# Optimization experiments

Hardware: AMD Instinct MI355X
Metric: run time of the kernel (lower is better)

The kernel has to match this reference:

```python
import jax, jax.numpy as jnp
import numpy as np

D = 512       # input_dim
K = 8         # output_size (number of bilinear slices)
L = 64        # hash_length
Q = 4096      # number of query vectors
C = 4096      # number of class vectors


def setup_inputs() -> dict:
    key = jax.random.key(0)
    ks = jax.random.split(key, 8)
    class_vector = jax.random.normal(ks[0], (C, D), dtype=jnp.float32)
    query_vector = jax.random.normal(ks[1], (Q, D), dtype=jnp.float32)
    # xavier_normal over (D, D, K): std = sqrt(2 / (fan_in + fan_out))
    xav = float(np.sqrt(2.0 / (D + D)))
    M = jax.random.normal(ks[2], (D, D, K), dtype=jnp.float32) * xav
    # score_layer: Linear(K, 1)
    lim_s = 1.0 / np.sqrt(K)
    score_w = jax.random.uniform(ks[3], (K,), jnp.float32, -lim_s, lim_s)
    score_b = jax.random.uniform(ks[4], (1,), jnp.float32, -lim_s, lim_s)
    # hash_layer: Linear(D, L) + Tanh
    lim_h = 1.0 / np.sqrt(D)
    hash_w = jax.random.uniform(ks[5], (L, D), jnp.float32, -lim_h, lim_h)
    hash_b = jax.random.uniform(ks[6], (L,), jnp.float32, -lim_h, lim_h)
    return {
        "class_vector": class_vector,
        "query_vector": query_vector,
        "M": M,
        "score_w": score_w,
        "score_b": score_b,
        "hash_w": hash_w,
        "hash_b": hash_b,
    }


def reference(class_vector, query_vector, M, score_w, score_b, hash_w, hash_b):
    # Looped bilinear product fused into one einsum:
    # inter_k = Q @ (C @ M[:,:,k]).T  ->  [Q, C, K]
    bi = jnp.einsum('ci,ijk,qj->qck', class_vector, M, query_vector)
    act = jax.nn.relu(bi)
    # score_layer: Linear(K, 1) then squeeze -> [Q, C]
    other = jnp.einsum('qck,k->qc', act, score_w) + score_b[0]
    relation_scores = jax.nn.softmax(other, axis=1)       # softmax over class dim
    query_features = relation_scores @ class_vector + query_vector  # [Q, D]
    hash_codes = jnp.tanh(query_features @ hash_w.T + hash_b)       # [Q, L]
    return hash_codes
```

## Files before the change

### kernel.cpp

```cpp
#include <hip/hip_runtime.h>
#include <hip/hip_bf16.h>
#include <math.h>

#define D_ 512
#define K_ 8
#define L_ 64
#define Q_ 4096
#define C_ 4096
#define N_ (C_ * K_)

typedef short short8 __attribute__((ext_vector_type(8)));
typedef float f32x4 __attribute__((ext_vector_type(4)));

static __device__ __forceinline__ void split2(float v, unsigned short& h, unsigned short& l) {
    __hip_bfloat16 hh = __float2bfloat16(v);
    float r = v - __bfloat162float(hh);
    __hip_bfloat16 ll = __float2bfloat16(r);
    h = *reinterpret_cast<unsigned short*>(&hh);
    l = *reinterpret_cast<unsigned short*>(&ll);
}

#define ASYNC_COPY16(gp, lp)                                                        \
    __builtin_amdgcn_global_load_lds((const __attribute__((address_space(1))) void*)(gp), \
                                     (__attribute__((address_space(3))) void*)(lp), \
                                     16, 0, 0)

__global__ void transpose_M_split(const float* __restrict__ M,
                                  unsigned short* __restrict__ Mh,
                                  unsigned short* __restrict__ Ml) {
    int idx = blockIdx.x * blockDim.x + threadIdx.x;
    int i = idx & (D_ - 1);
    int n2 = idx >> 9;
    int j = n2 & (D_ - 1);
    int k = n2 >> 9;
    float v = M[((size_t)i * D_ + j) * K_ + k];
    split2(v, Mh[idx], Ml[idx]);
}

__global__ void split_f32(const float* __restrict__ x,
                          unsigned short* __restrict__ hi,
                          unsigned short* __restrict__ lo) {
    int i = blockIdx.x * blockDim.x + threadIdx.x;
    split2(x[i], hi[i], lo[i]);
}

__global__ void transpose_split_classT(const float* __restrict__ x,
                                       unsigned short* __restrict__ Th,
                                       unsigned short* __restrict__ Tl) {
    int idx = blockIdx.x * blockDim.x + threadIdx.x;
    int c = idx & (C_ - 1);
    int d = idx >> 12;
    float v = x[(size_t)c * D_ + d];
    split2(v, Th[idx], Tl[idx]);
}

#define BM 128
#define BN 128
#define BNW 32
#define BKK 32

__device__ __forceinline__ void mfma_core(
    const unsigned short* __restrict__ Agh, const unsigned short* __restrict__ Agl,
    const unsigned short* __restrict__ Bgh, const unsigned short* __restrict__ Bgl,
    int lda, int ldb, int kd, int m0, int n0,
    unsigned short (*Ahb)[BM * BKK], unsigned short (*Alb)[BM * BKK],
    f32x4 acc[8][2]) {
    const int tid = threadIdx.x;
    const int lane = tid & 63;
    const int wid = tid >> 6;
    const int fr = lane & 15;
    const int fq = lane >> 4;
    const int co = (fq ^ ((fr >> 1) & 3)) * 8;

    const unsigned short* bh0 = Bgh + (size_t)(n0 + wid * BNW + fr) * ldb + fq * 8;
    const unsigned short* bl0 = Bgl + (size_t)(n0 + wid * BNW + fr) * ldb + fq * 8;

    short8 bh[2][2], bl[2][2];

#pragma unroll
    for (int h = 0; h < 2; ++h) {
        const int i2 = h * 256 + tid;
        const int r = i2 >> 2;
        const int cg = (i2 & 3) ^ ((r >> 1) & 3);
        const int ldsoff = (h * 256 + (tid & ~63)) * 8;
        const size_t go = (size_t)(m0 + r) * lda + cg * 8;
        ASYNC_COPY16(Agh + go, &Ahb[0][ldsoff]);
        ASYNC_COPY16(Agl + go, &Alb[0][ldsoff]);
    }
    bh[0][0] = *(const short8*)(bh0);
    bh[0][1] = *(const short8*)(bh0 + 16 * (size_t)ldb);
    bl[0][0] = *(const short8*)(bl0);
    bl[0][1] = *(const short8*)(bl0 + 16 * (size_t)ldb);
    __syncthreads();

    const int niter = kd / BKK;
#pragma unroll 2
    for (int it = 0; it < niter; ++it) {
        const int cur = it & 1, nxt = cur ^ 1;
        if (it + 1 < niter) {
            const int j0 = (it + 1) * BKK;
#pragma unroll
            for (int h = 0; h < 2; ++h) {
                const int i2 = h * 256 + tid;
                const int r = i2 >> 2;
                const int cg = (i2 & 3) ^ ((r >> 1) & 3);
                const int ldsoff = (h * 256 + (tid & ~63)) * 8;
                const size_t go = (size_t)(m0 + r) * lda + j0 + cg * 8;
                ASYNC_COPY16(Agh + go, &Ahb[nxt][ldsoff]);
                ASYNC_COPY16(Agl + go, &Alb[nxt][ldsoff]);
            }
            bh[nxt][0] = *(const short8*)(bh0 + j0);
            bh[nxt][1] = *(const short8*)(bh0 + 16 * (size_t)ldb + j0);
            bl[nxt][0] = *(const short8*)(bl0 + j0);
            bl[nxt][1] = *(const short8*)(bl0 + 16 * (size_t)ldb + j0);
        }
#pragma unroll
        for (int mi = 0; mi < 8; ++mi) {
            const short8 ah = *(const short8*)&Ahb[cur][(mi * 16 + fr) * BKK + co];
            const short8 al = *(const short8*)&Alb[cur][(mi * 16 + fr) * BKK + co];
#pragma unroll
            for (int ni = 0; ni < 2; ++ni) {
                acc[mi][ni] = __builtin_amdgcn_mfma_f32_16x16x32_bf16(ah, bh[cur][ni], acc[mi][ni], 0, 0, 0);
                acc[mi][ni] = __builtin_amdgcn_mfma_f32_16x16x32_bf16(ah, bl[cur][ni], acc[mi][ni], 0, 0, 0);
                acc[mi][ni] = __builtin_amdgcn_mfma_f32_16x16x32_bf16(al, bh[cur][ni], acc[mi][ni], 0, 0, 0);
            }
        }
        __syncthreads();
    }
}

#define CORE_PROLOGUE                                                            \
    __shared__ __attribute__((aligned(16))) unsigned short Ahb[2][BM * BKK];     \
    __shared__ __attribute__((aligned(16))) unsigned short Alb[2][BM * BKK];     \
    const int tid = threadIdx.x;                                                 \
    const int lane = tid & 63;                                                   \
    const int wid = tid >> 6;                                                    \
    const int fr = lane & 15;                                                    \
    const int fq = lane >> 4;                                                    \
    f32x4 acc[8][2] = {};                                                        \
    (void)tid;

__launch_bounds__(256, 4)
__global__ void gemm_P_mfma(const unsigned short* __restrict__ Chh,
                            const unsigned short* __restrict__ Cll,
                            const unsigned short* __restrict__ Mh,
                            const unsigned short* __restrict__ Ml,
                            unsigned short* __restrict__ Ph,
                            unsigned short* __restrict__ Pl) {
    CORE_PROLOGUE
    const int n0 = blockIdx.x * BN;
    const int c0 = blockIdx.y * BM;
    mfma_core(Chh, Cll, Mh, Ml, D_, D_, D_, c0, n0, Ahb, Alb, acc);
#pragma unroll
    for (int mi = 0; mi < 8; ++mi)
#pragma unroll
        for (int ni = 0; ni < 2; ++ni)
#pragma unroll
            for (int r = 0; r < 4; ++r) {
                int c = c0 + mi * 16 + fq * 4 + r;
                int n2 = n0 + wid * BNW + ni * 16 + fr;
                size_t o = (size_t)c * (K_ * D_) + n2;
                split2(acc[mi][ni][r], Ph[o], Pl[o]);
            }
}

__launch_bounds__(256, 4)
__global__ void bilinear_mfma(const unsigned short* __restrict__ Qh,
                              const unsigned short* __restrict__ Ql,
                              const unsigned short* __restrict__ Ph,
                              const unsigned short* __restrict__ Pl,
                              const float* __restrict__ sw,
                              const float* __restrict__ sb,
                              float* __restrict__ other) {
    CORE_PROLOGUE
    const int q0 = blockIdx.x * BM;
    const int n0 = blockIdx.y * BN;
    mfma_core(Qh, Ql, Ph, Pl, D_, D_, D_, q0, n0, Ahb, Alb, acc);
    const float wk = sw[lane & 7];
    const float bias = sb[0];
#pragma unroll
    for (int mi = 0; mi < 8; ++mi)
#pragma unroll
        for (int ni = 0; ni < 2; ++ni)
#pragma unroll
            for (int r = 0; r < 4; ++r) {
                float v = wk * fmaxf(acc[mi][ni][r], 0.f);
                v += __shfl_xor(v, 1);
                v += __shfl_xor(v, 2);
                v += __shfl_xor(v, 4);
                if ((lane & 7) == 0) {
                    int q = q0 + mi * 16 + fq * 4 + r;
                    int c = (n0 + wid * BNW + ni * 16 + fr) >> 3;
                    other[(size_t)q * C_ + c] = v + bias;
                }
            }
}

__launch_bounds__(256, 4)
__global__ void gemm_qf_mfma(const unsigned short* __restrict__ Sh,
                             const unsigned short* __restrict__ Sl,
                             const unsigned short* __restrict__ Th,
                             const unsigned short* __restrict__ Tl,
                             float* __restrict__ qfp_base) {
    CORE_PROLOGUE
    const int n0 = blockIdx.x * BN;
    const int q0 = blockIdx.y * BM;
    const int zoff = blockIdx.z * (C_ / 4);
    float* qfp = qfp_base + (size_t)blockIdx.z * Q_ * D_;
    mfma_core(Sh + zoff, Sl + zoff, Th + zoff, Tl + zoff,
              C_, C_, C_ / 4, q0, n0, Ahb, Alb, acc);
#pragma unroll
    for (int mi = 0; mi < 8; ++mi)
#pragma unroll
        for (int ni = 0; ni < 2; ++ni)
#pragma unroll
            for (int r = 0; r < 4; ++r) {
                int q = q0 + mi * 16 + fq * 4 + r;
                int d = n0 + wid * BNW + ni * 16 + fr;
                qfp[(size_t)q * D_ + d] = acc[mi][ni][r];
            }
}

__launch_bounds__(256)
__global__ void softmax_split(const float* __restrict__ other,
                              unsigned short* __restrict__ Sh,
                              unsigned short* __restrict__ Sl) {
    const int q = blockIdx.x;
    const float* row = other + (size_t)q * C_;
    const int tid = threadIdx.x;
    __shared__ float red[4];
    float v[16];
    float m = -1e30f;
#pragma unroll
    for (int it = 0; it < 16; ++it) {
        v[it] = row[tid + it * 256];
        m = fmaxf(m, v[it]);
    }
#pragma unroll
    for (int off = 32; off; off >>= 1) m = fmaxf(m, __shfl_down(m, off));
    if ((tid & 63) == 0) red[tid >> 6] = m;
    __syncthreads();
    m = fmaxf(fmaxf(red[0], red[1]), fmaxf(red[2], red[3]));
    __syncthreads();
    float s = 0.f;
#pragma unroll
    for (int it = 0; it < 16; ++it) {
        v[it] = __expf(v[it] - m);
        s += v[it];
    }
#pragma unroll
    for (int off = 32; off; off >>= 1) s += __shfl_down(s, off);
    if ((tid & 63) == 0) red[tid >> 6] = s;
    __syncthreads();
    const float inv = 1.f / (red[0] + red[1] + red[2] + red[3]);
#pragma unroll
    for (int it = 0; it < 16; ++it) {
        size_t o = (size_t)q * C_ + tid + it * 256;
        split2(v[it] * inv, Sh[o], Sl[o]);
    }
}

__launch_bounds__(256)
__global__ void hash_kernel(const float* __restrict__ qfp_base,
                            const float* __restrict__ Qv,
                            const float* __restrict__ hw,
                            const float* __restrict__ hb,
                            float* __restrict__ out) {
    __shared__ float sqf[4 * D_];
    const int q0 = blockIdx.x * 4;
    const int tid = threadIdx.x;
    {
        const float4* s0 = (const float4*)&qfp_base[(size_t)q0 * D_];
        const float4* s1 = (const float4*)&qfp_base[(size_t)Q_ * D_ + q0 * D_];
        const float4* s2 = (const float4*)&qfp_base[(size_t)2 * Q_ * D_ + q0 * D_];
        const float4* s3 = (const float4*)&qfp_base[(size_t)3 * Q_ * D_ + q0 * D_];
        const float4* s4 = (const float4*)&Qv[(size_t)q0 * D_];
        float4* dst = (float4*)sqf;
#pragma unroll
        for (int it = 0; it < 2; ++it) {
            int i = tid + it * 256;
            float4 a = s0[i], b = s1[i], c = s2[i], d = s3[i], e = s4[i];
            float4 o = {a.x + b.x + c.x + d.x + e.x, a.y + b.y + c.y + d.y + e.y,
                        a.z + b.z + c.z + d.z + e.z, a.w + b.w + c.w + d.w + e.w};
            dst[i] = o;
        }
    }
    __syncthreads();
    const int l = tid % L_;
    const int qi = tid / L_;
    float s = hb[l];
    const float* wrow = &hw[(size_t)l * D_];
    const float* xrow = &sqf[qi * D_];
#pragma unroll 4
    for (int d = 0; d < D_; d += 4) {
        float4 w4 = *(const float4*)&wrow[d];
        float4 x4 = *(const float4*)&xrow[d];
        s += x4.x * w4.x + x4.y * w4.y + x4.z * w4.z + x4.w * w4.w;
    }
    out[(size_t)(q0 + qi) * L_ + l] = tanhf(s);
}

extern "C" void kernel_launch(void* const* d_in, const int* in_sizes, int n_in,
                              void* d_out, int out_size, void* d_ws, size_t ws_size,
                              hipStream_t stream) {
    const float* class_v = (const float*)d_in[0];
    const float* query_v = (const float*)d_in[1];
    const float* M       = (const float*)d_in[2];
    const float* score_w = (const float*)d_in[3];
    const float* score_b = (const float*)d_in[4];
    const float* hash_w  = (const float*)d_in[5];
    const float* hash_b  = (const float*)d_in[6];
    float* out = (float*)d_out;

    char* base = (char*)d_ws;
    unsigned short* Ph = (unsigned short*)base;
    unsigned short* Pl = (unsigned short*)(base + (size_t)33554432);
    char* oreg          = base + (size_t)67108864;
    float* other        = (float*)oreg;
    unsigned short* Mh  = (unsigned short*)oreg;
    unsigned short* Ml  = (unsigned short*)(oreg + (size_t)4194304);
    unsigned short* Chh = (unsigned short*)(oreg + (size_t)8388608);
    unsigned short* Cll = (unsigned short*)(oreg + (size_t)12582912);
    float* qfp          = (float*)oreg;
    char* scratch = base + (size_t)134217728;
    unsigned short* Qh = (unsigned short*)scratch;
    unsigned short* Ql = (unsigned short*)(scratch + (size_t)4194304);
    unsigned short* Th = (unsigned short*)scratch;
    unsigned short* Tl = (unsigned short*)(scratch + (size_t)4194304);
    unsigned short* Sh = Ph;
    unsigned short* Sl = Pl;

    transpose_M_split<<<(K_ * D_ * D_) / 256, 256, 0, stream>>>(M, Mh, Ml);
    split_f32<<<(C_ * D_) / 256, 256, 0, stream>>>(class_v, Chh, Cll);
    split_f32<<<(Q_ * D_) / 256, 256, 0, stream>>>(query_v, Qh, Ql);
    gemm_P_mfma<<<dim3((K_ * D_) / BN, C_ / BM), 256, 0, stream>>>(Chh, Cll, Mh, Ml, Ph, Pl);
    bilinear_mfma<<<dim3(Q_ / BM, N_ / BN), 256, 0, stream>>>(Qh, Ql, Ph, Pl,
                                                              score_w, score_b, other);
    softmax_split<<<Q_, 256, 0, stream>>>(other, Sh, Sl);
    transpose_split_classT<<<(C_ * D_) / 256, 256, 0, stream>>>(class_v, Th, Tl);
    gemm_qf_mfma<<<dim3(D_ / BN, Q_ / BM, 4), 256, 0, stream>>>(Sh, Sl, Th, Tl, qfp);
    hash_kernel<<<Q_ / 4, 256, 0, stream>>>(qfp, query_v, hash_w, hash_b, out);
}
```

Measured before the change: 758.9 us.

## Switch GEMM core to 32x32x16 MFMA with 2x2 warp tiling

```diff
diff --git a/kernel.cpp b/kernel.cpp
--- a/kernel.cpp
+++ b/kernel.cpp
@@ -10,7 +10,7 @@
 #define N_ (C_ * K_)
 
 typedef short short8 __attribute__((ext_vector_type(8)));
-typedef float f32x4 __attribute__((ext_vector_type(4)));
+typedef float f32x16 __attribute__((ext_vector_type(16)));
 
 static __device__ __forceinline__ void split2(float v, unsigned short& h, unsigned short& l) {
     __hip_bfloat16 hh = __float2bfloat16(v);
@@ -56,7 +56,6 @@
 
 #define BM 128
 #define BN 128
-#define BNW 32
 #define BKK 32
 
 __device__ __forceinline__ void mfma_core(
@@ -64,33 +63,45 @@
     const unsigned short* __restrict__ Bgh, const unsigned short* __restrict__ Bgl,
     int lda, int ldb, int kd, int m0, int n0,
     unsigned short (*Ahb)[BM * BKK], unsigned short (*Alb)[BM * BKK],
-    f32x4 acc[8][2]) {
+    f32x16 acc[2][2]) {
     const int tid = threadIdx.x;
     const int lane = tid & 63;
     const int wid = tid >> 6;
-    const int fr = lane & 15;
-    const int fq = lane >> 4;
-    const int co = (fq ^ ((fr >> 1) & 3)) * 8;
-
-    const unsigned short* bh0 = Bgh + (size_t)(n0 + wid * BNW + fr) * ldb + fq * 8;
-    const unsigned short* bl0 = Bgl + (size_t)(n0 + wid * BNW + fr) * ldb + fq * 8;
-
-    short8 bh[2][2], bl[2][2];
-
-#pragma unroll
-    for (int h = 0; h < 2; ++h) {
-        const int i2 = h * 256 + tid;
-        const int r = i2 >> 2;
-        const int cg = (i2 & 3) ^ ((r >> 1) & 3);
-        const int ldsoff = (h * 256 + (tid & ~63)) * 8;
-        const size_t go = (size_t)(m0 + r) * lda + cg * 8;
-        ASYNC_COPY16(Agh + go, &Ahb[0][ldsoff]);
-        ASYNC_COPY16(Agl + go, &Alb[0][ldsoff]);
-    }
-    bh[0][0] = *(const short8*)(bh0);
-    bh[0][1] = *(const short8*)(bh0 + 16 * (size_t)ldb);
-    bl[0][0] = *(const short8*)(bl0);
-    bl[0][1] = *(const short8*)(bl0 + 16 * (size_t)ldb);
+    const int wr = (wid >> 1) * 64;
+    const int wc = (wid & 1) * 64;
+    const int r32 = lane & 31;
+    const int kh = lane >> 5;
+
+    const unsigned short* bbh = Bgh + (size_t)(n0 + wc + r32) * ldb + kh * 8;
+    const unsigned short* bbl = Bgl + (size_t)(n0 + wc + r32) * ldb + kh * 8;
+
+    short8 bh[2][2][2], bl[2][2][2];
+
+    auto stageA = [&](int buf, int j0) {
+#pragma unroll
+        for (int h = 0; h < 2; ++h) {
+            const int i2 = h * 256 + tid;
+            const int r = i2 >> 2;
+            const int cg = (i2 & 3) ^ ((r >> 1) & 3);
+            const int ldsoff = (h * 256 + (tid & ~63)) * 8;
+            const size_t go = (size_t)(m0 + r) * lda + j0 + cg * 8;
+            ASYNC_COPY16(Agh + go, &Ahb[buf][ldsoff]);
+            ASYNC_COPY16(Agl + go, &Alb[buf][ldsoff]);
+        }
+    };
+    auto loadB = [&](int buf, int j0) {
+#pragma unroll
+        for (int ni = 0; ni < 2; ++ni)
+#pragma unroll
+            for (int ks = 0; ks < 2; ++ks) {
+                const size_t off = (size_t)ni * 32 * ldb + j0 + ks * 16;
+                bh[buf][ni][ks] = *(const short8*)(bbh + off);
+                bl[buf][ni][ks] = *(const short8*)(bbl + off);
+            }
+    };
+
+    stageA(0, 0);
+    loadB(0, 0);
     __syncthreads();
 
     const int niter = kd / BKK;
@@ -98,32 +109,27 @@
     for (int it = 0; it < niter; ++it) {
         const int cur = it & 1, nxt = cur ^ 1;
         if (it + 1 < niter) {
-            const int j0 = (it + 1) * BKK;
-#pragma unroll
-            for (int h = 0; h < 2; ++h) {
-                const int i2 = h * 256 + tid;
-                const int r = i2 >> 2;
-                const int cg = (i2 & 3) ^ ((r >> 1) & 3);
-                const int ldsoff = (h * 256 + (tid & ~63)) * 8;
-                const size_t go = (size_t)(m0 + r) * lda + j0 + cg * 8;
-                ASYNC_COPY16(Agh + go, &Ahb[nxt][ldsoff]);
-                ASYNC_COPY16(Agl + go, &Alb[nxt][ldsoff]);
-            }
-            bh[nxt][0] = *(const short8*)(bh0 + j0);
-            bh[nxt][1] = *(const short8*)(bh0 + 16 * (size_t)ldb + j0);
-            bl[nxt][0] = *(const short8*)(bl0 + j0);
-            bl[nxt][1] = *(const short8*)(bl0 + 16 * (size_t)ldb + j0);
+            stageA(nxt, (it + 1) * BKK);
+            loadB(nxt, (it + 1) * BKK);
         }
 #pragma unroll
-        for (int mi = 0; mi < 8; ++mi) {
-            const short8 ah = *(const short8*)&Ahb[cur][(mi * 16 + fr) * BKK + co];
-            const short8 al = *(const short8*)&Alb[cur][(mi * 16 + fr) * BKK + co];
-#pragma unroll
-            for (int ni = 0; ni < 2; ++ni) {
-                acc[mi][ni] = __builtin_amdgcn_mfma_f32_16x16x32_bf16(ah, bh[cur][ni], acc[mi][ni], 0, 0, 0);
-                acc[mi][ni] = __builtin_amdgcn_mfma_f32_16x16x32_bf16(ah, bl[cur][ni], acc[mi][ni], 0, 0, 0);
-                acc[mi][ni] = __builtin_amdgcn_mfma_f32_16x16x32_bf16(al, bh[cur][ni], acc[mi][ni], 0, 0, 0);
-            }
+        for (int ks = 0; ks < 2; ++ks) {
+            short8 ah[2], al[2];
+#pragma unroll
+            for (int mi = 0; mi < 2; ++mi) {
+                const int row = wr + mi * 32 + r32;
+                const int cg = ((ks * 2 + kh) ^ ((row >> 1) & 3)) * 8;
+                ah[mi] = *(const short8*)&Ahb[cur][row * BKK + cg];
+                al[mi] = *(const short8*)&Alb[cur][row * BKK + cg];
+            }
+#pragma unroll
+            for (int mi = 0; mi < 2; ++mi)
+#pragma unroll
+                for (int ni = 0; ni < 2; ++ni) {
+                    acc[mi][ni] = __builtin_amdgcn_mfma_f32_32x32x16_bf16(ah[mi], bh[cur][ni][ks], acc[mi][ni], 0, 0, 0);
+                    acc[mi][ni] = __builtin_amdgcn_mfma_f32_32x32x16_bf16(ah[mi], bl[cur][ni][ks], acc[mi][ni], 0, 0, 0);
+                    acc[mi][ni] = __builtin_amdgcn_mfma_f32_32x32x16_bf16(al[mi], bh[cur][ni][ks], acc[mi][ni], 0, 0, 0);
+                }
         }
         __syncthreads();
     }
@@ -135,12 +141,15 @@
     const int tid = threadIdx.x;                                                 \
     const int lane = tid & 63;                                                   \
     const int wid = tid >> 6;                                                    \
-    const int fr = lane & 15;                                                    \
-    const int fq = lane >> 4;                                                    \
-    f32x4 acc[8][2] = {};                                                        \
+    const int wr = (wid >> 1) * 64;                                              \
+    const int wc = (wid & 1) * 64;                                               \
+    const int r32 = lane & 31;                                                   \
+    f32x16 acc[2][2] = {};                                                       \
     (void)tid;
 
-__launch_bounds__(256, 4)
+#define CD_ROW(reg) (((reg) & 3) + 8 * ((reg) >> 2) + 4 * (lane >> 5))
+
+__launch_bounds__(256, 3)
 __global__ void gemm_P_mfma(const unsigned short* __restrict__ Chh,
                             const unsigned short* __restrict__ Cll,
                             const unsigned short* __restrict__ Mh,
@@ -152,19 +161,19 @@
     const int c0 = blockIdx.y * BM;
     mfma_core(Chh, Cll, Mh, Ml, D_, D_, D_, c0, n0, Ahb, Alb, acc);
 #pragma unroll
-    for (int mi = 0; mi < 8; ++mi)
+    for (int mi = 0; mi < 2; ++mi)
 #pragma unroll
         for (int ni = 0; ni < 2; ++ni)
 #pragma unroll
-            for (int r = 0; r < 4; ++r) {
-                int c = c0 + mi * 16 + fq * 4 + r;
-                int n2 = n0 + wid * BNW + ni * 16 + fr;
+            for (int reg = 0; reg < 16; ++reg) {
+                int c = c0 + wr + mi * 32 + CD_ROW(reg);
+                int n2 = n0 + wc + ni * 32 + r32;
                 size_t o = (size_t)c * (K_ * D_) + n2;
-                split2(acc[mi][ni][r], Ph[o], Pl[o]);
-            }
-}
-
-__launch_bounds__(256, 4)
+                split2(acc[mi][ni][reg], Ph[o], Pl[o]);
+            }
+}
+
+__launch_bounds__(256, 3)
 __global__ void bilinear_mfma(const unsigned short* __restrict__ Qh,
                               const unsigned short* __restrict__ Ql,
                               const unsigned short* __restrict__ Ph,
@@ -179,24 +188,24 @@
     const float wk = sw[lane & 7];
     const float bias = sb[0];
 #pragma unroll
-    for (int mi = 0; mi < 8; ++mi)
+    for (int mi = 0; mi < 2; ++mi)
 #pragma unroll
         for (int ni = 0; ni < 2; ++ni)
 #pragma unroll
-            for (int r = 0; r < 4; ++r) {
-                float v = wk * fmaxf(acc[mi][ni][r], 0.f);
+            for (int reg = 0; reg < 16; ++reg) {
+                float v = wk * fmaxf(acc[mi][ni][reg], 0.f);
                 v += __shfl_xor(v, 1);
                 v += __shfl_xor(v, 2);
                 v += __shfl_xor(v, 4);
                 if ((lane & 7) == 0) {
-                    int q = q0 + mi * 16 + fq * 4 + r;
-                    int c = (n0 + wid * BNW + ni * 16 + fr) >> 3;
+                    int q = q0 + wr + mi * 32 + CD_ROW(reg);
+                    int c = (n0 + wc + ni * 32 + r32) >> 3;
                     other[(size_t)q * C_ + c] = v + bias;
                 }
             }
 }
 
-__launch_bounds__(256, 4)
+__launch_bounds__(256, 3)
 __global__ void gemm_qf_mfma(const unsigned short* __restrict__ Sh,
                              const unsigned short* __restrict__ Sl,
                              const unsigned short* __restrict__ Th,
@@ -210,14 +219,14 @@
     mfma_core(Sh + zoff, Sl + zoff, Th + zoff, Tl + zoff,
               C_, C_, C_ / 4, q0, n0, Ahb, Alb, acc);
 #pragma unroll
-    for (int mi = 0; mi < 8; ++mi)
+    for (int mi = 0; mi < 2; ++mi)
 #pragma unroll
         for (int ni = 0; ni < 2; ++ni)
 #pragma unroll
-            for (int r = 0; r < 4; ++r) {
-                int q = q0 + mi * 16 + fq * 4 + r;
-                int d = n0 + wid * BNW + ni * 16 + fr;
-                qfp[(size_t)q * D_ + d] = acc[mi][ni][r];
+            for (int reg = 0; reg < 16; ++reg) {
+                int q = q0 + wr + mi * 32 + CD_ROW(reg);
+                int d = n0 + wc + ni * 32 + r32;
+                qfp[(size_t)q * D_ + d] = acc[mi][ni][reg];
             }
 }
 
```

After: 951.2 us. 25.3% more time.

## Triple-buffer A tiles in LDS with one barrier per iteration in MFMA core

Applied to the files above, without the earlier changes.

```diff
diff --git a/kernel.cpp b/kernel.cpp
--- a/kernel.cpp
+++ b/kernel.cpp
@@ -77,61 +77,60 @@
 
     short8 bh[2][2], bl[2][2];
 
-#pragma unroll
-    for (int h = 0; h < 2; ++h) {
-        const int i2 = h * 256 + tid;
-        const int r = i2 >> 2;
-        const int cg = (i2 & 3) ^ ((r >> 1) & 3);
-        const int ldsoff = (h * 256 + (tid & ~63)) * 8;
-        const size_t go = (size_t)(m0 + r) * lda + cg * 8;
-        ASYNC_COPY16(Agh + go, &Ahb[0][ldsoff]);
-        ASYNC_COPY16(Agl + go, &Alb[0][ldsoff]);
-    }
-    bh[0][0] = *(const short8*)(bh0);
-    bh[0][1] = *(const short8*)(bh0 + 16 * (size_t)ldb);
-    bl[0][0] = *(const short8*)(bl0);
-    bl[0][1] = *(const short8*)(bl0 + 16 * (size_t)ldb);
-    __syncthreads();
+    auto stageA = [&](int buf, int j0) {
+#pragma unroll
+        for (int h = 0; h < 2; ++h) {
+            const int i2 = h * 256 + tid;
+            const int r = i2 >> 2;
+            const int cg = (i2 & 3) ^ ((r >> 1) & 3);
+            const int ldsoff = (h * 256 + (tid & ~63)) * 8;
+            const size_t go = (size_t)(m0 + r) * lda + j0 + cg * 8;
+            ASYNC_COPY16(Agh + go, &Ahb[buf][ldsoff]);
+            ASYNC_COPY16(Agl + go, &Alb[buf][ldsoff]);
+        }
+    };
+    auto loadB = [&](int buf, int j0) {
+        bh[buf][0] = *(const short8*)(bh0 + j0);
+        bh[buf][1] = *(const short8*)(bh0 + 16 * (size_t)ldb + j0);
+        bl[buf][0] = *(const short8*)(bl0 + j0);
+        bl[buf][1] = *(const short8*)(bl0 + 16 * (size_t)ldb + j0);
+    };
+
+    stageA(0, 0);
+    loadB(0, 0);
+    stageA(1, BKK);
 
     const int niter = kd / BKK;
-#pragma unroll 2
+    int cura = 0;
     for (int it = 0; it < niter; ++it) {
-        const int cur = it & 1, nxt = cur ^ 1;
+        const int curb = it & 1;
         if (it + 1 < niter) {
-            const int j0 = (it + 1) * BKK;
-#pragma unroll
-            for (int h = 0; h < 2; ++h) {
-                const int i2 = h * 256 + tid;
-                const int r = i2 >> 2;
-                const int cg = (i2 & 3) ^ ((r >> 1) & 3);
-                const int ldsoff = (h * 256 + (tid & ~63)) * 8;
-                const size_t go = (size_t)(m0 + r) * lda + j0 + cg * 8;
-                ASYNC_COPY16(Agh + go, &Ahb[nxt][ldsoff]);
-                ASYNC_COPY16(Agl + go, &Alb[nxt][ldsoff]);
-            }
-            bh[nxt][0] = *(const short8*)(bh0 + j0);
-            bh[nxt][1] = *(const short8*)(bh0 + 16 * (size_t)ldb + j0);
-            bl[nxt][0] = *(const short8*)(bl0 + j0);
-            bl[nxt][1] = *(const short8*)(bl0 + 16 * (size_t)ldb + j0);
+            asm volatile("s_waitcnt vmcnt(4)" ::: "memory");
+        } else {
+            asm volatile("s_waitcnt vmcnt(0)" ::: "memory");
         }
+        __builtin_amdgcn_s_barrier();
+        asm volatile("" ::: "memory");
+        if (it + 1 < niter) loadB(curb ^ 1, (it + 1) * BKK);
+        if (it + 2 < niter) stageA(cura == 0 ? 2 : cura - 1, (it + 2) * BKK);
 #pragma unroll
         for (int mi = 0; mi < 8; ++mi) {
-            const short8 ah = *(const short8*)&Ahb[cur][(mi * 16 + fr) * BKK + co];
-            const short8 al = *(const short8*)&Alb[cur][(mi * 16 + fr) * BKK + co];
+            const short8 ah = *(const short8*)&Ahb[cura][(mi * 16 + fr) * BKK + co];
+            const short8 al = *(const short8*)&Alb[cura][(mi * 16 + fr) * BKK + co];
 #pragma unroll
             for (int ni = 0; ni < 2; ++ni) {
-                acc[mi][ni] = __builtin_amdgcn_mfma_f32_16x16x32_bf16(ah, bh[cur][ni], acc[mi][ni], 0, 0, 0);
-                acc[mi][ni] = __builtin_amdgcn_mfma_f32_16x16x32_bf16(ah, bl[cur][ni], acc[mi][ni], 0, 0, 0);
-                acc[mi][ni] = __builtin_amdgcn_mfma_f32_16x16x32_bf16(al, bh[cur][ni], acc[mi][ni], 0, 0, 0);
+                acc[mi][ni] = __builtin_amdgcn_mfma_f32_16x16x32_bf16(ah, bh[curb][ni], acc[mi][ni], 0, 0, 0);
+                acc[mi][ni] = __builtin_amdgcn_mfma_f32_16x16x32_bf16(ah, bl[curb][ni], acc[mi][ni], 0, 0, 0);
+                acc[mi][ni] = __builtin_amdgcn_mfma_f32_16x16x32_bf16(al, bh[curb][ni], acc[mi][ni], 0, 0, 0);
             }
         }
-        __syncthreads();
+        cura = (cura == 2) ? 0 : cura + 1;
     }
 }
 
 #define CORE_PROLOGUE                                                            \
-    __shared__ __attribute__((aligned(16))) unsigned short Ahb[2][BM * BKK];     \
-    __shared__ __attribute__((aligned(16))) unsigned short Alb[2][BM * BKK];     \
+    __shared__ __attribute__((aligned(16))) unsigned short Ahb[3][BM * BKK];     \
+    __shared__ __attribute__((aligned(16))) unsigned short Alb[3][BM * BKK];     \
     const int tid = threadIdx.x;                                                 \
     const int lane = tid & 63;                                                   \
     const int wid = tid >> 6;                                                    \
@@ -140,7 +139,7 @@
     f32x4 acc[8][2] = {};                                                        \
     (void)tid;
 
-__launch_bounds__(256, 4)
+__launch_bounds__(256, 3)
 __global__ void gemm_P_mfma(const unsigned short* __restrict__ Chh,
                             const unsigned short* __restrict__ Cll,
                             const unsigned short* __restrict__ Mh,
@@ -164,7 +163,7 @@
             }
 }
 
-__launch_bounds__(256, 4)
+__launch_bounds__(256, 3)
 __global__ void bilinear_mfma(const unsigned short* __restrict__ Qh,
                               const unsigned short* __restrict__ Ql,
                               const unsigned short* __restrict__ Ph,
@@ -196,7 +195,7 @@
             }
 }
 
-__launch_bounds__(256, 4)
+__launch_bounds__(256, 3)
 __global__ void gemm_qf_mfma(const unsigned short* __restrict__ Sh,
                              const unsigned short* __restrict__ Sl,
                              const unsigned short* __restrict__ Th,
```

After: 1.261 ms. +66.2%, slower.
